# Performance work log

Hardware: AMD Instinct MI355X
Metric: run time of the kernel (lower is better)

Reference implementation:

```python
import jax, jax.numpy as jnp
import numpy as np

B, N, E, C, H = 2, 50000, 800000, 128, 512  # batch, nodes, edges, feat, 4*feat


def setup_inputs() -> dict:
    key = jax.random.key(0)
    ks = jax.random.split(key, 11)
    s_in = 1.0 / np.sqrt(C)
    s_h = 1.0 / np.sqrt(H)
    return {
        "graph_sig": jax.random.normal(ks[0], (B, N, C), dtype=jnp.float32),
        "edge_index": jax.random.randint(ks[1], (2, E), 0, N, dtype=jnp.int64),
        "W1_0": jax.random.normal(ks[2], (C, H), dtype=jnp.float32) * s_in,
        "b1_0": jnp.zeros((H,), dtype=jnp.float32),
        "W2_0": jax.random.normal(ks[3], (H, C), dtype=jnp.float32) * s_h,
        "b2_0": jnp.zeros((C,), dtype=jnp.float32),
        "W1_1": jax.random.normal(ks[4], (C, H), dtype=jnp.float32) * s_in,
        "b1_1": jnp.zeros((H,), dtype=jnp.float32),
        "W2_1": jax.random.normal(ks[5], (H, C), dtype=jnp.float32) * s_h,
        "b2_1": jnp.zeros((C,), dtype=jnp.float32),
    }


def gin_layer(x, src, dst, W1, b1, W2, b2):
    # GINConv with eps=0: h_i = MLP((1+eps)*x_i + sum_{j->i} x_j)
    # gather source features along edges, scatter-add into destinations
    agg = jnp.zeros_like(x).at[:, dst, :].add(x[:, src, :])  # (B, N, C)
    h = agg + x
    h = jax.nn.relu(jnp.einsum('bnc,ch->bnh', h, W1) + b1)
    return jnp.einsum('bnh,hc->bnc', h, W2) + b2


def reference(graph_sig, edge_index, W1_0, b1_0, W2_0, b2_0, W1_1, b1_1, W2_1, b2_1):
    src, dst = edge_index[0], edge_index[1]
    x = gin_layer(graph_sig, src, dst, W1_0, b1_0, W2_0, b2_0)
    x = gin_layer(x, src, dst, W1_1, b1_1, W2_1, b2_1)
    return x
```

## Files before the change

### kernel.cpp

```cpp
#include <hip/hip_runtime.h>

#define CDIM 128
#define HDIM 512
#define NB 2
#define NNODES 50000
#define NEDGES 800000
#define ROWS (NB * NNODES)

typedef _Float16 half8 __attribute__((ext_vector_type(8)));
typedef _Float16 half4 __attribute__((ext_vector_type(4)));
typedef float f32x4 __attribute__((ext_vector_type(4)));

__device__ __forceinline__ f32x4 mfma_f16(half8 a, half8 b, f32x4 c) {
  return __builtin_amdgcn_mfma_f32_16x16x32_f16(a, b, c, 0, 0, 0);
}

#define GLOAD_LDS16(g, l)                                                      \
  __builtin_amdgcn_global_load_lds(                                            \
      (const __attribute__((address_space(1))) void*)(g),                      \
      (__attribute__((address_space(3))) void*)(l), 16, 0, 0)

__global__ void hist_k(const int* __restrict__ ei, int* __restrict__ counts) {
  int e = blockIdx.x * 256 + threadIdx.x;
  if (e < NEDGES) atomicAdd(&counts[ei[NEDGES + e]], 1);
}

__global__ __launch_bounds__(1024) void scan_k(const int* __restrict__ counts,
                                               int* __restrict__ offsets,
                                               int* __restrict__ cursor) {
  __shared__ int sm[1024];
  __shared__ int carry;
  if (threadIdx.x == 0) carry = 0;
  __syncthreads();
  for (int base = 0; base < NNODES; base += 4096) {
    int i0 = base + threadIdx.x * 4;
    int v[4];
#pragma unroll
    for (int k = 0; k < 4; ++k) v[k] = (i0 + k < NNODES) ? counts[i0 + k] : 0;
    int s = v[0] + v[1] + v[2] + v[3];
    sm[threadIdx.x] = s;
    __syncthreads();
    for (int off = 1; off < 1024; off <<= 1) {
      int t = (threadIdx.x >= off) ? sm[threadIdx.x - off] : 0;
      __syncthreads();
      sm[threadIdx.x] += t;
      __syncthreads();
    }
    int run = carry + sm[threadIdx.x] - s;
#pragma unroll
    for (int k = 0; k < 4; ++k) {
      if (i0 + k < NNODES) {
        offsets[i0 + k] = run;
        cursor[i0 + k] = run;
      }
      run += v[k];
    }
    __syncthreads();
    if (threadIdx.x == 1023) carry += sm[1023];
    __syncthreads();
  }
  if (threadIdx.x == 0) offsets[NNODES] = NEDGES;
}

__global__ void fill_k(const int* __restrict__ ei, int* __restrict__ cursor,
                       int* __restrict__ col) {
  int e = blockIdx.x * 256 + threadIdx.x;
  if (e < NEDGES) {
    int d = ei[NEDGES + e];
    int p = atomicAdd(&cursor[d], 1);
    col[p] = ei[e];
  }
}

__global__ void cvt16i_k(const float* __restrict__ s, _Float16* __restrict__ d) {
  const int PB = NNODES * CDIM;
  int i = blockIdx.x * 256 + threadIdx.x;
  int str = gridDim.x * 256;
  for (; i < ROWS * (CDIM / 8); i += str) {
    size_t flat = (size_t)i * 8;
    int b = (int)(flat / PB);
    size_t r = flat - (size_t)b * PB;
    int n = (int)(r >> 7);
    int c0 = (int)(r & 127);
    float4 f0 = *(const float4*)(s + flat);
    float4 f1 = *(const float4*)(s + flat + 4);
    half8 o;
    o[0] = (_Float16)f0.x; o[1] = (_Float16)f0.y;
    o[2] = (_Float16)f0.z; o[3] = (_Float16)f0.w;
    o[4] = (_Float16)f1.x; o[5] = (_Float16)f1.y;
    o[6] = (_Float16)f1.z; o[7] = (_Float16)f1.w;
    *(half8*)(d + ((size_t)n * 2 + b) * CDIM + c0) = o;
  }
}

__global__ __launch_bounds__(256) void aggi_k(const _Float16* __restrict__ x,
                                              const int* __restrict__ offs,
                                              const int* __restrict__ col,
                                              _Float16* __restrict__ h) {
  int node = blockIdx.x * 4 + (threadIdx.x >> 6);
  int lane = threadIdx.x & 63;
  if (node >= NNODES) return;
  const half4* xp = (const half4*)x;
  half4 self = xp[(size_t)node * 64 + lane];
  float a0 = (float)self[0], a1 = (float)self[1], a2 = (float)self[2], a3 = (float)self[3];
  int e0 = offs[node], e1 = offs[node + 1];
  int e = e0;
  for (; e + 3 < e1; e += 4) {
    int s0 = col[e], s1 = col[e + 1], s2 = col[e + 2], s3 = col[e + 3];
    half4 v0 = xp[(size_t)s0 * 64 + lane];
    half4 v1 = xp[(size_t)s1 * 64 + lane];
    half4 v2 = xp[(size_t)s2 * 64 + lane];
    half4 v3 = xp[(size_t)s3 * 64 + lane];
    a0 += (float)v0[0] + (float)v1[0] + (float)v2[0] + (float)v3[0];
    a1 += (float)v0[1] + (float)v1[1] + (float)v2[1] + (float)v3[1];
    a2 += (float)v0[2] + (float)v1[2] + (float)v2[2] + (float)v3[2];
    a3 += (float)v0[3] + (float)v1[3] + (float)v2[3] + (float)v3[3];
  }
  for (; e < e1; ++e) {
    int s0 = col[e];
    half4 v0 = xp[(size_t)s0 * 64 + lane];
    a0 += (float)v0[0];
    a1 += (float)v0[1];
    a2 += (float)v0[2];
    a3 += (float)v0[3];
  }
  half4 r;
  r[0] = (_Float16)a0; r[1] = (_Float16)a1;
  r[2] = (_Float16)a2; r[3] = (_Float16)a3;
  ((half4*)h)[(size_t)node * 64 + lane] = r;
}

__global__ void pack_mlp(const float* __restrict__ W1, const float* __restrict__ W2,
                         _Float16* __restrict__ dst) {
  int tid = blockIdx.x * 256 + threadIdx.x;
  if (tid >= 16384) return;
  int l = tid & 63;
  int g = (tid >> 6) & 7;
  int c = (tid >> 9) & 15;
  int isW2 = tid >> 13;
  int lg = l >> 4, l15 = l & 15;
  _Float16* o;
  if (!isW2) {
    int jt = g >> 2, ks = g & 3;
    int k0 = ks * 32 + lg * 8;
    int n = c * 32 + jt * 16 + l15;
    o = dst + (size_t)c * 8192 + g * 512 + l * 8;
#pragma unroll
    for (int i = 0; i < 8; ++i) o[i] = (_Float16)W1[(size_t)(k0 + i) * HDIM + n];
  } else {
    int k0 = c * 32 + lg * 8;
    int n = g * 16 + l15;
    o = dst + (size_t)c * 8192 + 4096 + g * 512 + l * 8;
#pragma unroll
    for (int i = 0; i < 8; ++i) o[i] = (_Float16)W2[(size_t)(k0 + i) * CDIM + n];
  }
}

template <typename OT, bool REMAP>
__global__ __launch_bounds__(256, 4) void mlp_v3(
    const _Float16* __restrict__ hin, const _Float16* __restrict__ wpk,
    const float* __restrict__ b1, const float* __restrict__ b2,
    OT* __restrict__ out) {
  __shared__ alignas(16) _Float16 wbuf[2][8192];
  __shared__ alignas(16) _Float16 tbuf[4][32 * 32];

  const int tidx = threadIdx.x;
  const int lane = tidx & 63;
  const int wid = tidx >> 6;
  const int l15 = lane & 15, lg = lane >> 4;
  const long long r0 = (long long)blockIdx.x * 128 + wid * 32;

  half8 A[2][4];
#pragma unroll
  for (int rt = 0; rt < 2; ++rt) {
    long long row = r0 + rt * 16 + l15;
    if (row >= ROWS) row = ROWS - 1;
    const _Float16* hp = hin + row * CDIM + lg * 8;
#pragma unroll
    for (int ks = 0; ks < 4; ++ks) A[rt][ks] = *(const half8*)(hp + ks * 32);
  }

  {
    const _Float16* src = wpk;
#pragma unroll
    for (int q = 0; q < 4; ++q) {
      int s = wid * 4 + q;
      GLOAD_LDS16(src + s * 512 + lane * 8, &wbuf[0][s * 512]);
    }
  }
  __syncthreads();

  f32x4 acc[2][8];
#pragma unroll
  for (int rt = 0; rt < 2; ++rt)
#pragma unroll
    for (int ct = 0; ct < 8; ++ct) acc[rt][ct] = (f32x4){0.f, 0.f, 0.f, 0.f};

  _Float16* tw = &tbuf[wid][0];

  for (int c = 0; c < 16; ++c) {
    const int cur = c & 1;
    if (c + 1 < 16) {
      const _Float16* src = wpk + (size_t)(c + 1) * 8192;
#pragma unroll
      for (int q = 0; q < 4; ++q) {
        int s = wid * 4 + q;
        GLOAD_LDS16(src + s * 512 + lane * 8, &wbuf[cur ^ 1][s * 512]);
      }
    }
    const _Float16* w1c = &wbuf[cur][0];
    const _Float16* w2c = &wbuf[cur][4096];

#pragma unroll
    for (int jt = 0; jt < 2; ++jt) {
      f32x4 t0 = (f32x4){0.f, 0.f, 0.f, 0.f};
      f32x4 t1 = (f32x4){0.f, 0.f, 0.f, 0.f};
#pragma unroll
      for (int ks = 0; ks < 4; ++ks) {
        half8 b = *(const half8*)(w1c + (jt * 4 + ks) * 512 + lane * 8);
        t0 = mfma_f16(A[0][ks], b, t0);
        t1 = mfma_f16(A[1][ks], b, t1);
      }
      float bb = b1[c * 32 + jt * 16 + l15];
      int j = jt * 16 + l15;
#pragma unroll
      for (int r = 0; r < 4; ++r) {
        int n0 = lg * 4 + r;
        tw[n0 * 32 + (j ^ (((n0 >> 2) & 3) << 3))] = (_Float16)fmaxf(t0[r] + bb, 0.f);
        int n1 = 16 + lg * 4 + r;
        tw[n1 * 32 + (j ^ (((n1 >> 2) & 3) << 3))] = (_Float16)fmaxf(t1[r] + bb, 0.f);
      }
    }

    half8 ta0, ta1;
    {
      int n = l15;
      ta0 = *(const half8*)(tw + n * 32 + ((lg * 8) ^ (((n >> 2) & 3) << 3)));
      n = 16 + l15;
      ta1 = *(const half8*)(tw + n * 32 + ((lg * 8) ^ (((n >> 2) & 3) << 3)));
    }
#pragma unroll
    for (int ct = 0; ct < 8; ++ct) {
      half8 b = *(const half8*)(w2c + ct * 512 + lane * 8);
      acc[0][ct] = mfma_f16(ta0, b, acc[0][ct]);
      acc[1][ct] = mfma_f16(ta1, b, acc[1][ct]);
    }
    __syncthreads();
  }

#pragma unroll
  for (int ct = 0; ct < 8; ++ct) {
    float b2v = b2[ct * 16 + l15];
#pragma unroll
    for (int rt = 0; rt < 2; ++rt) {
#pragma unroll
      for (int r = 0; r < 4; ++r) {
        long long g = r0 + rt * 16 + lg * 4 + r;
        if (g < ROWS) {
          size_t off;
          if (REMAP) {
            off = (size_t)(g & 1) * NNODES * CDIM + (size_t)(g >> 1) * CDIM + ct * 16 + l15;
          } else {
            off = (size_t)g * CDIM + ct * 16 + l15;
          }
          out[off] = (OT)(acc[rt][ct][r] + b2v);
        }
      }
    }
  }
}

extern "C" void kernel_launch(void* const* d_in, const int* in_sizes, int n_in,
                              void* d_out, int out_size, void* d_ws, size_t ws_size,
                              hipStream_t stream) {
  const float* x0 = (const float*)d_in[0];
  const int* ei = (const int*)d_in[1];
  const float* W1_0 = (const float*)d_in[2];
  const float* b1_0 = (const float*)d_in[3];
  const float* W2_0 = (const float*)d_in[4];
  const float* b2_0 = (const float*)d_in[5];
  const float* W1_1 = (const float*)d_in[6];
  const float* b1_1 = (const float*)d_in[7];
  const float* W2_1 = (const float*)d_in[8];
  const float* b2_1 = (const float*)d_in[9];
  float* out = (float*)d_out;

  _Float16* xh = (_Float16*)d_ws;
  _Float16* hh = xh + (size_t)ROWS * CDIM;
  _Float16* wpk0 = hh + (size_t)ROWS * CDIM;
  _Float16* wpk1 = wpk0 + 131072;
  int* counts = (int*)(wpk1 + 131072);
  int* offsets = counts + NNODES;
  int* cursor = offsets + NNODES + 1;
  int* col = cursor + NNODES;

  const int eBlocks = (NEDGES + 255) / 256;
  const int aggBlocks = (NNODES + 3) / 4;
  const int mlpBlocks = (ROWS + 127) / 128;

  hipMemsetAsync(counts, 0, NNODES * sizeof(int), stream);
  hist_k<<<eBlocks, 256, 0, stream>>>(ei, counts);
  scan_k<<<1, 1024, 0, stream>>>(counts, offsets, cursor);
  fill_k<<<eBlocks, 256, 0, stream>>>(ei, cursor, col);

  pack_mlp<<<64, 256, 0, stream>>>(W1_0, W2_0, wpk0);
  pack_mlp<<<64, 256, 0, stream>>>(W1_1, W2_1, wpk1);

  cvt16i_k<<<2048, 256, 0, stream>>>(x0, xh);

  aggi_k<<<aggBlocks, 256, 0, stream>>>(xh, offsets, col, hh);
  mlp_v3<_Float16, false><<<mlpBlocks, 256, 0, stream>>>(hh, wpk0, b1_0, b2_0, xh);
  aggi_k<<<aggBlocks, 256, 0, stream>>>(xh, offsets, col, hh);
  mlp_v3<float, true><<<mlpBlocks, 256, 0, stream>>>(hh, wpk1, b1_1, b2_1, out);
}
```

Before: 367.6 us.

## Split prefix scan into multi-block passes and deepen aggregation gather unroll

The single-block serial scan over node degrees becomes a three-kernel scan: per-block sums, a tiny serial pass over 13 block bases, then a per-block local scan that writes offsets and cursor. The aggregation kernel now unrolls its gather by 8 with two independent accumulator sets, aiming for more memory loads in flight. The scan change adds two extra kernel launches and uses a little extra workspace after col. The unroll raises register use.

Measured after the change: 338.4 us. -8.0%, faster.

```diff
diff --git a/kernel.cpp b/kernel.cpp
--- a/kernel.cpp
+++ b/kernel.cpp
@@ -25,41 +25,67 @@
   if (e < NEDGES) atomicAdd(&counts[ei[NEDGES + e]], 1);
 }
 
-__global__ __launch_bounds__(1024) void scan_k(const int* __restrict__ counts,
+#define SC_BLOCKS 13
+
+__global__ __launch_bounds__(256) void scan1_k(const int* __restrict__ counts,
+                                               int* __restrict__ bsum) {
+  __shared__ int ws[4];
+  int i0 = blockIdx.x * 4096 + threadIdx.x * 16;
+  int s = 0;
+#pragma unroll
+  for (int k = 0; k < 16; ++k) {
+    int i = i0 + k;
+    s += (i < NNODES) ? counts[i] : 0;
+  }
+#pragma unroll
+  for (int off = 1; off < 64; off <<= 1) s += __shfl_down(s, off);
+  if ((threadIdx.x & 63) == 0) ws[threadIdx.x >> 6] = s;
+  __syncthreads();
+  if (threadIdx.x == 0) bsum[blockIdx.x] = ws[0] + ws[1] + ws[2] + ws[3];
+}
+
+__global__ void scan2_k(const int* __restrict__ bsum, int* __restrict__ bbase,
+                        int* __restrict__ offsets) {
+  int run = 0;
+  for (int b = 0; b < SC_BLOCKS; ++b) {
+    bbase[b] = run;
+    run += bsum[b];
+  }
+  offsets[NNODES] = run;
+}
+
+__global__ __launch_bounds__(256) void scan3_k(const int* __restrict__ counts,
+                                               const int* __restrict__ bbase,
                                                int* __restrict__ offsets,
                                                int* __restrict__ cursor) {
-  __shared__ int sm[1024];
-  __shared__ int carry;
-  if (threadIdx.x == 0) carry = 0;
+  __shared__ int sm[256];
+  int i0 = blockIdx.x * 4096 + threadIdx.x * 16;
+  int v[16];
+  int tsum = 0;
+#pragma unroll
+  for (int k = 0; k < 16; ++k) {
+    int i = i0 + k;
+    v[k] = (i < NNODES) ? counts[i] : 0;
+    tsum += v[k];
+  }
+  sm[threadIdx.x] = tsum;
   __syncthreads();
-  for (int base = 0; base < NNODES; base += 4096) {
-    int i0 = base + threadIdx.x * 4;
-    int v[4];
-#pragma unroll
-    for (int k = 0; k < 4; ++k) v[k] = (i0 + k < NNODES) ? counts[i0 + k] : 0;
-    int s = v[0] + v[1] + v[2] + v[3];
-    sm[threadIdx.x] = s;
+  for (int off = 1; off < 256; off <<= 1) {
+    int t = (threadIdx.x >= off) ? sm[threadIdx.x - off] : 0;
     __syncthreads();
-    for (int off = 1; off < 1024; off <<= 1) {
-      int t = (threadIdx.x >= off) ? sm[threadIdx.x - off] : 0;
-      __syncthreads();
-      sm[threadIdx.x] += t;
-      __syncthreads();
-    }
-    int run = carry + sm[threadIdx.x] - s;
-#pragma unroll
-    for (int k = 0; k < 4; ++k) {
-      if (i0 + k < NNODES) {
-        offsets[i0 + k] = run;
-        cursor[i0 + k] = run;
-      }
-      run += v[k];
-    }
+    sm[threadIdx.x] += t;
     __syncthreads();
-    if (threadIdx.x == 1023) carry += sm[1023];
-    __syncthreads();
-  }
-  if (threadIdx.x == 0) offsets[NNODES] = NEDGES;
+  }
+  int run = bbase[blockIdx.x] + sm[threadIdx.x] - tsum;
+#pragma unroll
+  for (int k = 0; k < 16; ++k) {
+    int i = i0 + k;
+    if (i < NNODES) {
+      offsets[i] = run;
+      cursor[i] = run;
+    }
+    run += v[k];
+  }
 }
 
 __global__ void fill_k(const int* __restrict__ ei, int* __restrict__ cursor,
@@ -103,30 +129,48 @@
   const half4* xp = (const half4*)x;
   half4 self = xp[(size_t)node * 64 + lane];
   float a0 = (float)self[0], a1 = (float)self[1], a2 = (float)self[2], a3 = (float)self[3];
-  int e0 = offs[node], e1 = offs[node + 1];
-  int e = e0;
-  for (; e + 3 < e1; e += 4) {
+  float c0 = 0.f, c1 = 0.f, c2 = 0.f, c3 = 0.f;
+  int e = offs[node], e1 = offs[node + 1];
+  for (; e + 7 < e1; e += 8) {
     int s0 = col[e], s1 = col[e + 1], s2 = col[e + 2], s3 = col[e + 3];
+    int s4 = col[e + 4], s5 = col[e + 5], s6 = col[e + 6], s7 = col[e + 7];
     half4 v0 = xp[(size_t)s0 * 64 + lane];
     half4 v1 = xp[(size_t)s1 * 64 + lane];
     half4 v2 = xp[(size_t)s2 * 64 + lane];
     half4 v3 = xp[(size_t)s3 * 64 + lane];
+    half4 v4 = xp[(size_t)s4 * 64 + lane];
+    half4 v5 = xp[(size_t)s5 * 64 + lane];
+    half4 v6 = xp[(size_t)s6 * 64 + lane];
+    half4 v7 = xp[(size_t)s7 * 64 + lane];
     a0 += (float)v0[0] + (float)v1[0] + (float)v2[0] + (float)v3[0];
     a1 += (float)v0[1] + (float)v1[1] + (float)v2[1] + (float)v3[1];
     a2 += (float)v0[2] + (float)v1[2] + (float)v2[2] + (float)v3[2];
     a3 += (float)v0[3] + (float)v1[3] + (float)v2[3] + (float)v3[3];
-  }
-  for (; e < e1; ++e) {
+    c0 += (float)v4[0] + (float)v5[0] + (float)v6[0] + (float)v7[0];
+    c1 += (float)v4[1] + (float)v5[1] + (float)v6[1] + (float)v7[1];
+    c2 += (float)v4[2] + (float)v5[2] + (float)v6[2] + (float)v7[2];
+    c3 += (float)v4[3] + (float)v5[3] + (float)v6[3] + (float)v7[3];
+  }
+  for (; e + 1 < e1; e += 2) {
+    int s0 = col[e], s1 = col[e + 1];
+    half4 v0 = xp[(size_t)s0 * 64 + lane];
+    half4 v1 = xp[(size_t)s1 * 64 + lane];
+    a0 += (float)v0[0]; a1 += (float)v0[1];
+    a2 += (float)v0[2]; a3 += (float)v0[3];
+    c0 += (float)v1[0]; c1 += (float)v1[1];
+    c2 += (float)v1[2]; c3 += (float)v1[3];
+  }
+  if (e < e1) {
     int s0 = col[e];
     half4 v0 = xp[(size_t)s0 * 64 + lane];
-    a0 += (float)v0[0];
-    a1 += (float)v0[1];
-    a2 += (float)v0[2];
-    a3 += (float)v0[3];
+    a0 += (float)v0[0]; a1 += (float)v0[1];
+    a2 += (float)v0[2]; a3 += (float)v0[3];
   }
   half4 r;
-  r[0] = (_Float16)a0; r[1] = (_Float16)a1;
-  r[2] = (_Float16)a2; r[3] = (_Float16)a3;
+  r[0] = (_Float16)(a0 + c0);
+  r[1] = (_Float16)(a1 + c1);
+  r[2] = (_Float16)(a2 + c2);
+  r[3] = (_Float16)(a3 + c3);
   ((half4*)h)[(size_t)node * 64 + lane] = r;
 }
 
@@ -293,6 +337,8 @@
   int* offsets = counts + NNODES;
   int* cursor = offsets + NNODES + 1;
   int* col = cursor + NNODES;
+  int* bsum = col + NEDGES;
+  int* bbase = bsum + 16;
 
   const int eBlocks = (NEDGES + 255) / 256;
   const int aggBlocks = (NNODES + 3) / 4;
@@ -300,7 +346,9 @@
 
   hipMemsetAsync(counts, 0, NNODES * sizeof(int), stream);
   hist_k<<<eBlocks, 256, 0, stream>>>(ei, counts);
-  scan_k<<<1, 1024, 0, stream>>>(counts, offsets, cursor);
+  scan1_k<<<SC_BLOCKS, 256, 0, stream>>>(counts, bsum);
+  scan2_k<<<1, 1, 0, stream>>>(bsum, bbase, offsets);
+  scan3_k<<<SC_BLOCKS, 256, 0, stream>>>(counts, bbase, offsets, cursor);
   fill_k<<<eBlocks, 256, 0, stream>>>(ei, cursor, col);
 
   pack_mlp<<<64, 256, 0, stream>>>(W1_0, W2_0, wpk0);
```
